# Kernel tuning notes

Measured on AMD Instinct MI355X. Metric: run time of the kernel, lower is better.

Reference implementation:

```python
import jax, jax.numpy as jnp
import numpy as np
import math


def setup_inputs() -> dict:
    key = jax.random.key(0)
    kq, kk, kv, kt, kd = jax.random.split(key, 5)
    B, L, H, E = 2, 2048, 16, 64
    return {
        "queries": jax.random.normal(kq, (B, L, H, E), dtype=jnp.float32),
        "keys": jax.random.normal(kk, (B, L, H, E), dtype=jnp.float32),
        "values": jax.random.normal(kv, (B, L, H, E), dtype=jnp.float32),
        "tau": jax.random.uniform(kt, (B, 1), dtype=jnp.float32),
        "delta": jax.random.normal(kd, (B, L), dtype=jnp.float32),
    }


def reference(queries, keys, values, tau, delta):
    # queries/keys/values: [B, L, H, E]; tau: [B,1]; delta: [B,S]
    B, L, H, E = queries.shape
    scale = 1.0 / math.sqrt(E)
    # scores: [B, H, L, S]; tau broadcasts [B,1,1,1], delta broadcasts [B,1,1,S]
    scores = (jnp.einsum('blhe,bshe->bhls', queries, keys)
              * tau[:, None, None, :]
              + delta[:, None, None, :])
    # causal mask (mask_flag=True, attn_mask=None path)
    causal = jnp.triu(jnp.ones((L, L), dtype=bool), k=1)
    scores = jnp.where(causal, -jnp.inf, scores)
    A = jax.nn.softmax(scale * scores, axis=-1)  # dropout p=0
    V = jnp.einsum('bhls,bshd->blhd', A, values)
    return V
```

## Files before the change

kernel.cpp:

```cpp
#include <hip/hip_runtime.h>
#include <math.h>

#define LL 2048
#define HH 16
#define EE 64
#define ROWSTR (HH*EE)
#define NBH 32
#define NQT 32
#define NST 32
#define SCALE 0.125f
#define LOG2E 1.4426950408889634f
#define TILE_SH 4096
#define KPRE_OFF 4096
#define TILES_TOTAL ((size_t)NBH * NST)
#define WS_NEED (16384ull + 2ull * TILES_TOTAL * TILE_SH * 2ull)

using bf16x8 = __attribute__((ext_vector_type(8))) __bf16;
using f32x4  = __attribute__((ext_vector_type(4))) float;
using s16x4  = __attribute__((ext_vector_type(4))) short;

__device__ __forceinline__ unsigned pkbf(float lo, float hi) {
    unsigned l = __builtin_bit_cast(unsigned, lo) + 0x8000u;
    unsigned h = __builtin_bit_cast(unsigned, hi) + 0x8000u;
    return __builtin_amdgcn_perm(h, l, 0x07060302u);
}
__device__ __forceinline__ uint4 pack8(float4 a, float4 b) {
    uint4 u; u.x = pkbf(a.x, a.y); u.y = pkbf(a.z, a.w);
    u.z = pkbf(b.x, b.y); u.w = pkbf(b.z, b.w); return u;
}

#if __has_builtin(__builtin_amdgcn_mfma_f32_16x16x16_bf16)
using bf16x4 = __attribute__((ext_vector_type(4))) __bf16;
__device__ __forceinline__ f32x4 mfma16(s16x4 a, s16x4 b, f32x4 c) {
    return __builtin_amdgcn_mfma_f32_16x16x16_bf16(
        __builtin_bit_cast(bf16x4, a), __builtin_bit_cast(bf16x4, b), c, 0, 0, 0);
}
#else
__device__ __forceinline__ f32x4 mfma16(s16x4 a, s16x4 b, f32x4 c) {
    return __builtin_amdgcn_mfma_f32_16x16x16bf16_1k(a, b, c, 0, 0, 0);
}
#endif

__device__ __forceinline__ void gl_lds16(const void* g, void* l) {
    __builtin_amdgcn_global_load_lds(
        (const __attribute__((address_space(1))) unsigned int*)(unsigned long long)g,
        (__attribute__((address_space(3))) unsigned int*)(unsigned long long)l,
        16, 0, 0);
}

__global__ __launch_bounds__(256) void dsprep(
    const float* __restrict__ K, const float* __restrict__ V,
    const float* __restrict__ delta, float* __restrict__ ws)
{
    const int bid = blockIdx.x;
    const int t = threadIdx.x;
    float* dsc = ws;
    unsigned short* kpre = (unsigned short*)(ws + KPRE_OFF);
    unsigned short* vpre = kpre + TILES_TOTAL * TILE_SH;

    if (bid >= NBH * NST) {
        const int i = (bid - NBH * NST) * 256 + t;
        dsc[i] = delta[i] * (SCALE * LOG2E);
        return;
    }
    const int bh = bid & 31, st = bid >> 5;
    const int b = bh >> 4, h = bh & 15;

    unsigned short* kimg = kpre + ((size_t)bh * NST + st) * TILE_SH;
    #pragma unroll
    for (int i = 0; i < 2; ++i) {
        const int slot = t + i * 256;
        const int k = slot >> 3, c = slot & 7;
        const float* src = K + ((size_t)(b * LL + st * 64 + k) * HH + h) * EE + c * 8;
        float4 a = ((const float4*)src)[0], bq = ((const float4*)src)[1];
        *(uint4*)&kimg[k * 64 + (c ^ (k & 7)) * 8] = pack8(a, bq);
    }

    __shared__ float vt[64 * 65];
    {
        const int s = t >> 2, seg = (t & 3) * 16;
        const float* src = V + ((size_t)(b * LL + st * 64 + s) * HH + h) * EE + seg;
        #pragma unroll
        for (int i = 0; i < 4; ++i) {
            float4 f = ((const float4*)src)[i];
            vt[s * 65 + seg + 4 * i + 0] = f.x;
            vt[s * 65 + seg + 4 * i + 1] = f.y;
            vt[s * 65 + seg + 4 * i + 2] = f.z;
            vt[s * 65 + seg + 4 * i + 3] = f.w;
        }
    }
    __syncthreads();
    {
        unsigned short* vimg = vpre + ((size_t)bh * NST + st) * TILE_SH;
        const int e = t >> 2, g = t & 3;
        unsigned u[8];
        #pragma unroll
        for (int A = 0; A < 4; ++A) {
            float x0 = vt[(16 * A + 4 * g + 0) * 65 + e];
            float x1 = vt[(16 * A + 4 * g + 1) * 65 + e];
            float x2 = vt[(16 * A + 4 * g + 2) * 65 + e];
            float x3 = vt[(16 * A + 4 * g + 3) * 65 + e];
            u[2 * A]     = pkbf(x0, x1);
            u[2 * A + 1] = pkbf(x2, x3);
        }
        *(uint4*)&vimg[e * 64 + ((2 * g)     ^ (e & 7)) * 8] = uint4{u[0], u[1], u[2], u[3]};
        *(uint4*)&vimg[e * 64 + ((2 * g + 1) ^ (e & 7)) * 8] = uint4{u[4], u[5], u[6], u[7]};
    }
}

__global__ __launch_bounds__(256, 8) void dsattn_dma(
    const float* __restrict__ Qg, const float* __restrict__ taug,
    const float* __restrict__ ws_, float* __restrict__ Og)
{
    __shared__ __align__(16) unsigned short Ks[2][TILE_SH];
    __shared__ __align__(16) unsigned short Vt[2][TILE_SH];

    const int tid  = threadIdx.x;
    const int w    = tid >> 6;
    const int lane = tid & 63;
    const int m    = lane & 15;
    const int quad = lane >> 4;

    const int bid = blockIdx.x;
    const int bh  = bid & (NBH - 1);
    const int qt  = (NQT - 1) - (bid >> 5);
    const int b   = bh >> 4;
    const int h   = bh & 15;

    const float* dsc = ws_;
    const unsigned short* kpre = (const unsigned short*)(ws_ + KPRE_OFF);
    const unsigned short* vpre = kpre + TILES_TOTAL * TILE_SH;
    const unsigned short* ktiles = kpre + (size_t)bh * NST * TILE_SH;
    const unsigned short* vtiles = vpre + (size_t)bh * NST * TILE_SH;

    const float qscale = taug[b] * (SCALE * LOG2E);
    const int thr = w * 16 + m - quad * 4;

    bf16x8 qb[2];
    {
        const float* qp = Qg + ((size_t)(b * LL + qt * 64 + w * 16 + m) * HH + h) * EE + quad * 8;
        #pragma unroll
        for (int ch = 0; ch < 2; ++ch) {
            float4 f0 = *(const float4*)(qp + ch * 32);
            float4 f1 = *(const float4*)(qp + ch * 32 + 4);
            f0.x *= qscale; f0.y *= qscale; f0.z *= qscale; f0.w *= qscale;
            f1.x *= qscale; f1.y *= qscale; f1.z *= qscale; f1.w *= qscale;
            qb[ch] = __builtin_bit_cast(bf16x8, pack8(f0, f1));
        }
    }

    const float* dbase = dsc + b * LL + quad * 4;

    gl_lds16(ktiles + tid * 8,        &Ks[0][w * 512]);
    gl_lds16(ktiles + 2048 + tid * 8, &Ks[0][2048 + w * 512]);
    gl_lds16(vtiles + tid * 8,        &Vt[0][w * 512]);
    gl_lds16(vtiles + 2048 + tid * 8, &Vt[0][2048 + w * 512]);

    f32x4 Oacc[4] = {};
    float l_ = 0.f;

    for (int st = 0; st <= qt; ++st) {
        const int par = st & 1;
        const unsigned short* KsP = Ks[par];
        const unsigned short* VtP = Vt[par];

        __syncthreads();

        if (st < qt) {
            const unsigned short* kn = ktiles + (st + 1) * TILE_SH;
            const unsigned short* vn = vtiles + (st + 1) * TILE_SH;
            gl_lds16(kn + tid * 8,        &Ks[par ^ 1][w * 512]);
            gl_lds16(kn + 2048 + tid * 8, &Ks[par ^ 1][2048 + w * 512]);
            gl_lds16(vn + tid * 8,        &Vt[par ^ 1][w * 512]);
            gl_lds16(vn + 2048 + tid * 8, &Vt[par ^ 1][2048 + w * 512]);
        }

        const float* dp = dbase + st * 64;
        f32x4 S[4];
        S[0] = __builtin_bit_cast(f32x4, *(const float4*)(dp));
        S[1] = __builtin_bit_cast(f32x4, *(const float4*)(dp + 16));
        S[2] = __builtin_bit_cast(f32x4, *(const float4*)(dp + 32));
        S[3] = __builtin_bit_cast(f32x4, *(const float4*)(dp + 48));

        #pragma unroll
        for (int n = 0; n < 4; ++n) {
            bf16x8 kf = *(const bf16x8*)&KsP[(16 * n + m) * 64 + (quad ^ (m & 7)) * 8];
            S[n] = __builtin_amdgcn_mfma_f32_16x16x32_bf16(kf, qb[0], S[n], 0, 0, 0);
        }
        #pragma unroll
        for (int n = 0; n < 4; ++n) {
            bf16x8 kf = *(const bf16x8*)&KsP[(16 * n + m) * 64 + ((quad + 4) ^ (m & 7)) * 8];
            S[n] = __builtin_amdgcn_mfma_f32_16x16x32_bf16(kf, qb[1], S[n], 0, 0, 0);
        }

        if (st == qt) {
            #pragma unroll
            for (int n = 0; n < 4; ++n)
                #pragma unroll
                for (int r = 0; r < 4; ++r)
                    if (16 * n + r > thr) S[n][r] = -INFINITY;
        }

        float rs[4];
        #pragma unroll
        for (int n = 0; n < 4; ++n) {
            float p0 = __builtin_amdgcn_exp2f(S[n][0]);
            float p1 = __builtin_amdgcn_exp2f(S[n][1]);
            float p2 = __builtin_amdgcn_exp2f(S[n][2]);
            float p3 = __builtin_amdgcn_exp2f(S[n][3]);
            S[n][0] = p0; S[n][1] = p1; S[n][2] = p2; S[n][3] = p3;
            rs[n] = (p0 + p1) + (p2 + p3);
        }
        l_ += (rs[0] + rs[1]) + (rs[2] + rs[3]);

        s16x4 pb[4];
        #pragma unroll
        for (int n = 0; n < 4; ++n) {
            uint2 u; u.x = pkbf(S[n][0], S[n][1]); u.y = pkbf(S[n][2], S[n][3]);
            pb[n] = __builtin_bit_cast(s16x4, u);
        }

        #pragma unroll
        for (int eb = 0; eb < 4; ++eb) {
            const int e = 16 * eb + m;
            uint4 r0 = *(const uint4*)&VtP[e * 64 + ((2 * quad)     ^ (m & 7)) * 8];
            uint4 r1 = *(const uint4*)&VtP[e * 64 + ((2 * quad + 1) ^ (m & 7)) * 8];
            f32x4 o = Oacc[eb];
            o = mfma16(__builtin_bit_cast(s16x4, uint2{r0.x, r0.y}), pb[0], o);
            o = mfma16(__builtin_bit_cast(s16x4, uint2{r0.z, r0.w}), pb[1], o);
            o = mfma16(__builtin_bit_cast(s16x4, uint2{r1.x, r1.y}), pb[2], o);
            o = mfma16(__builtin_bit_cast(s16x4, uint2{r1.z, r1.w}), pb[3], o);
            Oacc[eb] = o;
        }
    }

    {
        float lt = l_ + __shfl_xor(l_, 16);
        lt = lt + __shfl_xor(lt, 32);
        const float inv = __builtin_amdgcn_rcpf(lt);
        float* op = Og + ((size_t)(b * LL + qt * 64 + w * 16 + m) * HH + h) * EE + quad * 4;
        #pragma unroll
        for (int n = 0; n < 4; ++n) {
            float4 o = {Oacc[n][0] * inv, Oacc[n][1] * inv, Oacc[n][2] * inv, Oacc[n][3] * inv};
            *(float4*)(op + 16 * n) = o;
        }
    }
}

__global__ __launch_bounds__(512, 4) void dsattn_reg(
    const float* __restrict__ Qg, const float* __restrict__ Kg,
    const float* __restrict__ Vg, const float* __restrict__ taug,
    const float* __restrict__ dg, float* __restrict__ Og)
{
    __shared__ __align__(16) unsigned short Ks[2][64 * 64];
    __shared__ __align__(16) unsigned short Vt[2][64 * 64];

    const int tid  = threadIdx.x;
    const int w    = tid >> 6;
    const int lane = tid & 63;
    const int m    = lane & 15;
    const int quad = lane >> 4;

    const int bid = blockIdx.x;
    const int bh  = bid & (NBH - 1);
    const int g   = bid >> 5;
    const int tt  = (g < 8) ? (15 - g) : (g - 8);
    const int b   = bh >> 4;
    const int h   = bh & 15;

    const float qscale = taug[b] * (SCALE * LOG2E);
    const float dscale = SCALE * LOG2E;
    const int diag_st = 2 * tt + (w >> 2);
    const int thr = (w & 3) * 16 + m - quad * 4;

    bf16x8 qb[2];
    {
        const float* qp = Qg + ((size_t)(b * LL + tt * 128 + w * 16 + m) * HH + h) * EE + quad * 8;
        #pragma unroll
        for (int ch = 0; ch < 2; ++ch) {
            float4 f0 = *(const float4*)(qp + ch * 32);
            float4 f1 = *(const float4*)(qp + ch * 32 + 4);
            f0.x *= qscale; f0.y *= qscale; f0.z *= qscale; f0.w *= qscale;
            f1.x *= qscale; f1.y *= qscale; f1.z *= qscale; f1.w *= qscale;
            qb[ch] = __builtin_bit_cast(bf16x8, pack8(f0, f1));
        }
    }

    const int skey = tid >> 3, kc = tid & 7, se0 = (tid & 7) * 8;
    const int sv = (tid & 31) * 2, ve = (tid >> 5) * 4;
    const float* kbase = Kg + ((size_t)b * LL * HH + h) * EE;
    const float* vbase = Vg + ((size_t)b * LL * HH + h) * EE;
    const float* dbase = dg + b * LL;
    const int nst = 2 * tt + 2;

    float4 kr0, kr1, va, vb, dr0, dr1, dr2, dr3;
    {
        const float* kp = kbase + (size_t)skey * ROWSTR + se0;
        kr0 = ((const float4*)kp)[0]; kr1 = ((const float4*)kp)[1];
        const float* vp = vbase + (size_t)sv * ROWSTR + ve;
        va = *(const float4*)(vp); vb = *(const float4*)(vp + ROWSTR);
        const float* dp = dbase + quad * 4;
        dr0 = *(const float4*)(dp); dr1 = *(const float4*)(dp + 16);
        dr2 = *(const float4*)(dp + 32); dr3 = *(const float4*)(dp + 48);
    }

    f32x4 Oacc[4] = {};
    float l_ = 0.f;

    for (int st = 0; st < nst; ++st) {
        const int par = st & 1;
        unsigned short* KsP = Ks[par];
        unsigned short* VtP = Vt[par];

        *(uint4*)&KsP[skey * 64 + (kc ^ (skey & 7)) * 8] = pack8(kr0, kr1);
        {
            float ra[4] = {va.x, va.y, va.z, va.w};
            float rb[4] = {vb.x, vb.y, vb.z, vb.w};
            #pragma unroll
            for (int i = 0; i < 4; ++i) {
                const int e = ve + i;
                *(unsigned*)&VtP[e * 64 + (((sv >> 3) ^ (e & 7)) * 8) + (sv & 7)] = pkbf(ra[i], rb[i]);
            }
        }
        __syncthreads();

        f32x4 dvx[4];
        dvx[0] = f32x4{dr0.x * dscale, dr0.y * dscale, dr0.z * dscale, dr0.w * dscale};
        dvx[1] = f32x4{dr1.x * dscale, dr1.y * dscale, dr1.z * dscale, dr1.w * dscale};
        dvx[2] = f32x4{dr2.x * dscale, dr2.y * dscale, dr2.z * dscale, dr2.w * dscale};
        dvx[3] = f32x4{dr3.x * dscale, dr3.y * dscale, dr3.z * dscale, dr3.w * dscale};

        if (st + 1 < nst) {
            const int row = (st + 1) * 64;
            const float* kp = kbase + (size_t)(row + skey) * ROWSTR + se0;
            kr0 = ((const float4*)kp)[0]; kr1 = ((const float4*)kp)[1];
            const float* vp = vbase + (size_t)(row + sv) * ROWSTR + ve;
            va = *(const float4*)(vp); vb = *(const float4*)(vp + ROWSTR);
            const float* dp = dbase + row + quad * 4;
            dr0 = *(const float4*)(dp); dr1 = *(const float4*)(dp + 16);
            dr2 = *(const float4*)(dp + 32); dr3 = *(const float4*)(dp + 48);
        }

        if (st <= diag_st) {
            f32x4 S[4];
            #pragma unroll
            for (int n = 0; n < 4; ++n) {
                bf16x8 kf = *(const bf16x8*)&KsP[(16 * n + m) * 64 + (quad ^ (m & 7)) * 8];
                S[n] = __builtin_amdgcn_mfma_f32_16x16x32_bf16(kf, qb[0], dvx[n], 0, 0, 0);
            }
            #pragma unroll
            for (int n = 0; n < 4; ++n) {
                bf16x8 kf = *(const bf16x8*)&KsP[(16 * n + m) * 64 + ((quad + 4) ^ (m & 7)) * 8];
                S[n] = __builtin_amdgcn_mfma_f32_16x16x32_bf16(kf, qb[1], S[n], 0, 0, 0);
            }
            if (st == diag_st) {
                #pragma unroll
                for (int n = 0; n < 4; ++n)
                    #pragma unroll
                    for (int r = 0; r < 4; ++r)
                        if (16 * n + r > thr) S[n][r] = -INFINITY;
            }
            float rs[4];
            #pragma unroll
            for (int n = 0; n < 4; ++n) {
                float p0 = __builtin_amdgcn_exp2f(S[n][0]);
                float p1 = __builtin_amdgcn_exp2f(S[n][1]);
                float p2 = __builtin_amdgcn_exp2f(S[n][2]);
                float p3 = __builtin_amdgcn_exp2f(S[n][3]);
                S[n][0] = p0; S[n][1] = p1; S[n][2] = p2; S[n][3] = p3;
                rs[n] = (p0 + p1) + (p2 + p3);
            }
            l_ += (rs[0] + rs[1]) + (rs[2] + rs[3]);

            s16x4 pb[4];
            #pragma unroll
            for (int n = 0; n < 4; ++n) {
                uint2 u; u.x = pkbf(S[n][0], S[n][1]); u.y = pkbf(S[n][2], S[n][3]);
                pb[n] = __builtin_bit_cast(s16x4, u);
            }
            #pragma unroll
            for (int eb = 0; eb < 4; ++eb) {
                const int e = 16 * eb + m;
                s16x4 vf[4];
                #pragma unroll
                for (int n = 0; n < 4; ++n)
                    vf[n] = *(const s16x4*)&VtP[e * 64 + (((2 * n + (quad >> 1)) ^ (m & 7)) * 8) + (quad & 1) * 4];
                #pragma unroll
                for (int n = 0; n < 4; ++n)
                    Oacc[eb] = mfma16(vf[n], pb[n], Oacc[eb]);
            }
        }
    }

    {
        float lt = l_ + __shfl_xor(l_, 16);
        lt = lt + __shfl_xor(lt, 32);
        const float inv = __builtin_amdgcn_rcpf(lt);
        float* op = Og + ((size_t)(b * LL + tt * 128 + w * 16 + m) * HH + h) * EE + quad * 4;
        #pragma unroll
        for (int n = 0; n < 4; ++n) {
            float4 o = {Oacc[n][0] * inv, Oacc[n][1] * inv, Oacc[n][2] * inv, Oacc[n][3] * inv};
            *(float4*)(op + 16 * n) = o;
        }
    }
}

extern "C" void kernel_launch(void* const* d_in, const int* in_sizes, int n_in,
                              void* d_out, int out_size, void* d_ws, size_t ws_size,
                              hipStream_t stream) {
    const float* Q     = (const float*)d_in[0];
    const float* K     = (const float*)d_in[1];
    const float* V     = (const float*)d_in[2];
    const float* tau   = (const float*)d_in[3];
    const float* delta = (const float*)d_in[4];
    float* out = (float*)d_out;
    float* ws  = (float*)d_ws;
    if (ws_size >= WS_NEED) {
        dsprep<<<dim3(NBH * NST + 16), dim3(256), 0, stream>>>(K, V, delta, ws);
        dsattn_dma<<<dim3(NBH * NQT), dim3(256), 0, stream>>>(Q, tau, ws, out);
    } else {
        dsattn_reg<<<dim3(NBH * (NQT / 2)), dim3(512), 0, stream>>>(Q, K, V, tau, delta, out);
    }
}
```

Before: 127.4 us.

## Split long causal query tiles across two blocks and combine partial results

Query tiles in the upper half (qt>=16) are split into two blocks, each covering half of the key tiles, so work per block is more uniform and the tail of the causal triangle finishes sooner. Each half writes unnormalized partial outputs and row sums to workspace, and a new combine kernel adds them and normalizes. The split relies on no max-subtraction in the softmax, so the partial sums add directly. This costs an extra kernel launch, extra workspace traffic for the partial outputs, and a larger workspace requirement that could force the fallback path if the workspace is too small.

```diff
diff --git a/kernel.cpp b/kernel.cpp
--- a/kernel.cpp
+++ b/kernel.cpp
@@ -13,7 +13,14 @@
 #define TILE_SH 4096
 #define KPRE_OFF 4096
 #define TILES_TOTAL ((size_t)NBH * NST)
-#define WS_NEED (16384ull + 2ull * TILES_TOTAL * TILE_SH * 2ull)
+#define IMG_FLOATS (TILES_TOTAL * TILE_SH / 2)
+#define PPART 2097152
+#define LPART 32768
+#define P0_OFF (KPRE_OFF + 2 * IMG_FLOATS)
+#define P1_OFF (P0_OFF + PPART)
+#define L0_OFF (P1_OFF + PPART)
+#define L1_OFF (L0_OFF + LPART)
+#define WS_NEED ((size_t)(L1_OFF + LPART) * 4)
 
 using bf16x8 = __attribute__((ext_vector_type(8))) __bf16;
 using f32x4  = __attribute__((ext_vector_type(4))) float;
@@ -110,7 +117,7 @@
 
 __global__ __launch_bounds__(256, 8) void dsattn_dma(
     const float* __restrict__ Qg, const float* __restrict__ taug,
-    const float* __restrict__ ws_, float* __restrict__ Og)
+    float* __restrict__ ws_, float* __restrict__ Og)
 {
     __shared__ __align__(16) unsigned short Ks[2][TILE_SH];
     __shared__ __align__(16) unsigned short Vt[2][TILE_SH];
@@ -122,10 +129,24 @@
     const int quad = lane >> 4;
 
     const int bid = blockIdx.x;
-    const int bh  = bid & (NBH - 1);
-    const int qt  = (NQT - 1) - (bid >> 5);
-    const int b   = bh >> 4;
-    const int h   = bh & 15;
+    int qt, bh, half, is_split;
+    if (bid < 1024) {
+        is_split = 1;
+        qt   = (NQT - 1) - (bid >> 6);
+        half = (bid >> 5) & 1;
+        bh   = bid & 31;
+    } else {
+        is_split = 0;
+        const int j = bid - 1024;
+        qt   = 15 - (j >> 5);
+        half = 0;
+        bh   = j & 31;
+    }
+    const int b = bh >> 4;
+    const int h = bh & 15;
+    const int mid = (qt + 1) >> 1;
+    const int s_begin = (is_split && half) ? mid : 0;
+    const int s_end   = (is_split && !half) ? mid : (qt + 1);
 
     const float* dsc = ws_;
     const unsigned short* kpre = (const unsigned short*)(ws_ + KPRE_OFF);
@@ -151,22 +172,26 @@
 
     const float* dbase = dsc + b * LL + quad * 4;
 
-    gl_lds16(ktiles + tid * 8,        &Ks[0][w * 512]);
-    gl_lds16(ktiles + 2048 + tid * 8, &Ks[0][2048 + w * 512]);
-    gl_lds16(vtiles + tid * 8,        &Vt[0][w * 512]);
-    gl_lds16(vtiles + 2048 + tid * 8, &Vt[0][2048 + w * 512]);
+    {
+        const unsigned short* k0 = ktiles + s_begin * TILE_SH;
+        const unsigned short* v0 = vtiles + s_begin * TILE_SH;
+        gl_lds16(k0 + tid * 8,        &Ks[0][w * 512]);
+        gl_lds16(k0 + 2048 + tid * 8, &Ks[0][2048 + w * 512]);
+        gl_lds16(v0 + tid * 8,        &Vt[0][w * 512]);
+        gl_lds16(v0 + 2048 + tid * 8, &Vt[0][2048 + w * 512]);
+    }
 
     f32x4 Oacc[4] = {};
     float l_ = 0.f;
 
-    for (int st = 0; st <= qt; ++st) {
-        const int par = st & 1;
+    for (int st = s_begin; st < s_end; ++st) {
+        const int par = (st - s_begin) & 1;
         const unsigned short* KsP = Ks[par];
         const unsigned short* VtP = Vt[par];
 
         __syncthreads();
 
-        if (st < qt) {
+        if (st + 1 < s_end) {
             const unsigned short* kn = ktiles + (st + 1) * TILE_SH;
             const unsigned short* vn = vtiles + (st + 1) * TILE_SH;
             gl_lds16(kn + tid * 8,        &Ks[par ^ 1][w * 512]);
@@ -237,14 +262,44 @@
     {
         float lt = l_ + __shfl_xor(l_, 16);
         lt = lt + __shfl_xor(lt, 32);
-        const float inv = __builtin_amdgcn_rcpf(lt);
-        float* op = Og + ((size_t)(b * LL + qt * 64 + w * 16 + m) * HH + h) * EE + quad * 4;
-        #pragma unroll
-        for (int n = 0; n < 4; ++n) {
-            float4 o = {Oacc[n][0] * inv, Oacc[n][1] * inv, Oacc[n][2] * inv, Oacc[n][3] * inv};
-            *(float4*)(op + 16 * n) = o;
-        }
-    }
+        if (is_split) {
+            const int rowIdx = (qt - 16) * 64 + w * 16 + m;
+            float* P = ws_ + (half ? P1_OFF : P0_OFF)
+                     + ((size_t)(b * 1024 + rowIdx) * HH + h) * EE + quad * 4;
+            #pragma unroll
+            for (int n = 0; n < 4; ++n) {
+                float4 o = {Oacc[n][0], Oacc[n][1], Oacc[n][2], Oacc[n][3]};
+                *(float4*)(P + 16 * n) = o;
+            }
+            if (quad == 0)
+                ws_[(half ? L1_OFF : L0_OFF) + (b * 1024 + rowIdx) * HH + h] = lt;
+        } else {
+            const float inv = __builtin_amdgcn_rcpf(lt);
+            float* op = Og + ((size_t)(b * LL + qt * 64 + w * 16 + m) * HH + h) * EE + quad * 4;
+            #pragma unroll
+            for (int n = 0; n < 4; ++n) {
+                float4 o = {Oacc[n][0] * inv, Oacc[n][1] * inv, Oacc[n][2] * inv, Oacc[n][3] * inv};
+                *(float4*)(op + 16 * n) = o;
+            }
+        }
+    }
+}
+
+__global__ __launch_bounds__(256) void dscombine(
+    const float* __restrict__ ws, float* __restrict__ out)
+{
+    const unsigned gid = blockIdx.x * 256 + threadIdx.x;
+    const float4* O0 = (const float4*)(ws + P0_OFF);
+    const float4* O1 = (const float4*)(ws + P1_OFF);
+    const float* l0 = ws + L0_OFF;
+    const float* l1 = ws + L1_OFF;
+    const unsigned j = gid >> 4;
+    const float inv = __builtin_amdgcn_rcpf(l0[j] + l1[j]);
+    float4 a = O0[gid], c = O1[gid];
+    float4 o = {(a.x + c.x) * inv, (a.y + c.y) * inv,
+                (a.z + c.z) * inv, (a.w + c.w) * inv};
+    const size_t outF4 = (size_t)gid + ((size_t)(gid >> 18) + 1) * 262144;
+    ((float4*)out)[outF4] = o;
 }
 
 __global__ __launch_bounds__(512, 4) void dsattn_reg(
@@ -417,7 +472,8 @@
     float* ws  = (float*)d_ws;
     if (ws_size >= WS_NEED) {
         dsprep<<<dim3(NBH * NST + 16), dim3(256), 0, stream>>>(K, V, delta, ws);
-        dsattn_dma<<<dim3(NBH * NQT), dim3(256), 0, stream>>>(Q, tau, ws, out);
+        dsattn_dma<<<dim3(1536), dim3(256), 0, stream>>>(Q, tau, ws, out);
+        dscombine<<<dim3(PPART / 4 / 256), dim3(256), 0, stream>>>(ws, out);
     } else {
         dsattn_reg<<<dim3(NBH * (NQT / 2)), dim3(512), 0, stream>>>(Q, K, V, tau, delta, out);
     }
```

New measurement: 135.7 us. +6.5%, slower.
